# Performance work log

Hardware: AMD Instinct MI355X
Metric: run time of the kernel (lower is better)

Reference implementation:

```python
import jax, jax.numpy as jnp
import numpy as np

B, H, W, C = 512, 7, 7, 768


def _conv3(v, k, b):
    # 1-channel conv1d, kernel size 3, padding 1. v: (B, L), k: (3,), b: scalar
    vp = jnp.pad(v, ((0, 0), (1, 1)))
    return k[0] * vp[:, :-2] + k[1] * vp[:, 1:-1] + k[2] * vp[:, 2:] + b


def setup_inputs() -> dict:
    key = jax.random.key(0)
    ks = jax.random.split(key, 32)
    n = lambda i, shape, s=0.02: jax.random.normal(ks[i], shape, dtype=jnp.float32) * s
    inp = {
        "x": jax.random.normal(ks[0], (B, H, W, C), dtype=jnp.float32),
        # 1x1 Conv2d(dim,dim) weights stored as (out,in)
        "Wh": n(1, (C, C)), "bh": n(2, (C,)),
        "Ww": n(3, (C, C)), "bw": n(4, (C,)),
        "Ws": n(5, (C, C)), "bs": n(6, (C,)),
        # Conv1d(1,1,1) -> scalar weight/bias
        "convH_w": n(7, ()), "convH_b": n(8, ()),
        "convH2_k": n(9, (3,)), "convH2_b": n(10, ()),
        # Conv1d(2,1,1)
        "mixhw_k": n(11, (2,)), "mixhw_b": n(12, ()),
        "mixhw2_k": n(13, (3,)), "mixhw2_b": n(14, ()),
        # Conv1d(3,1,1)
        "mixhws_k": n(15, (3,)), "mixhws_b": n(16, ()),
        "mixhws2_k": n(17, (3,)), "mixhws2_b": n(18, ()),
        # Linear(7, dim)
        "linH_W": n(19, (C, 7), 0.1), "linH_b": n(20, (C,)),
        "linW_W": n(21, (C, 7), 0.1), "linW_b": n(22, (C,)),
        # mix_all: Conv2d(3*dim, dim, 1)
        "mixall_W": n(23, (C, 3 * C)), "mixall_b": n(24, (C,)),
        # proj: Linear(dim, dim)
        "proj_W": n(25, (C, C)), "proj_b": n(26, (C,)),
        "gate_weights": jnp.ones((2,), dtype=jnp.float32),
    }
    return inp


def reference(x, Wh, bh, Ww, bw, Ws, bs, convH_w, convH_b, convH2_k, convH2_b,
              mixhw_k, mixhw_b, mixhw2_k, mixhw2_b, mixhws_k, mixhws_b,
              mixhws2_k, mixhws2_b, linH_W, linH_b, linW_W, linW_b,
              mixall_W, mixall_b, proj_W, proj_b, gate_weights):
    gelu = lambda v: jax.nn.gelu(v, approximate=False)
    sig = jax.nn.sigmoid
    add = x

    # H branch: mlp_h (1x1 conv over channels), pool over (W, C) per H index
    h = gelu(jnp.einsum('bhwc,dc->bhwd', x, Wh) + bh)          # (B,H,W,C)
    h2v = h.mean(axis=(2, 3))                                   # (B,H)
    g_h = sig(_conv3(sig(h2v * convH_w + convH_b), convH2_k, convH2_b))  # (B,H)
    h3 = h * g_h[:, :, None, None]                              # gate per H index

    # W branch: pool over (H, C) per W index, gate mixed with H stats
    w = gelu(jnp.einsum('bhwc,dc->bhwd', x, Ww) + bw)           # (B,H,W,C)
    w2v = w.mean(axis=(1, 3))                                   # (B,W)
    g_hw = sig(_conv3(sig(mixhw_k[0] * h2v + mixhw_k[1] * w2v + mixhw_b),
                      mixhw2_k, mixhw2_b))                      # (B,W)
    w3 = w * g_hw[:, None, :, None]                             # gate per W index

    # C branch: pool over (H, W) per channel, gate mixed with lifted H/W stats
    s = gelu(jnp.einsum('bhwc,dc->bhwd', x, Ws) + bs)           # (B,H,W,C)
    s1v = s.mean(axis=(1, 2))                                   # (B,C)
    h2l = h2v @ linH_W.T + linH_b                               # (B,C)
    w2l = w2v @ linW_W.T + linW_b                               # (B,C)
    g_c = sig(_conv3(sig(mixhws_k[0] * h2l + mixhws_k[1] * w2l
                         + mixhws_k[2] * s1v + mixhws_b),
                     mixhws2_k, mixhws2_b))                     # (B,C)
    s2 = s * g_c[:, None, None, :]                              # gate per channel

    # concat along channel dim + 1x1 mixing conv + proj
    cat = jnp.concatenate([h3, w3, s2], axis=-1)                # (B,H,W,3C)
    mixed = jnp.einsum('bhwk,dk->bhwd', cat, mixall_W) + mixall_b
    out = mixed @ proj_W.T + proj_b
    out = out * gate_weights[0] + add * gate_weights[1]
    return out
```

## Files before the change

### kernel.cpp

```cpp
#include <hip/hip_runtime.h>
#include <cstdint>
#include <cstddef>

typedef __attribute__((ext_vector_type(8))) __bf16 bf16x8;
typedef __attribute__((ext_vector_type(4))) float f32x4;

__device__ __forceinline__ float sigm(float v) { return 1.0f / (1.0f + expf(-v)); }

__device__ __forceinline__ float gelu_fast(float v) {
  float u = v * (1.0f + 0.044715f * v * v);
  float z = 1.5957691216057308f * u;
  return v / (1.0f + __expf(-z));
}

__device__ __forceinline__ void async16(__bf16* lds, const __bf16* g) {
  __builtin_amdgcn_global_load_lds(
      (const __attribute__((address_space(1))) void*)g,
      (__attribute__((address_space(3))) void*)lds, 16, 0, 0);
}

__global__ __launch_bounds__(256) void k_convert(const float* __restrict__ src,
                                                 __bf16* __restrict__ dst, int n8) {
  int i = blockIdx.x * 256 + threadIdx.x;
  if (i >= n8) return;
  const f32x4* s4 = (const f32x4*)src;
  f32x4 a = s4[2 * i], b = s4[2 * i + 1];
  bf16x8 o;
#pragma unroll
  for (int e = 0; e < 4; ++e) { o[e] = (__bf16)a[e]; o[4 + e] = (__bf16)b[e]; }
  ((bf16x8*)dst)[i] = o;
}

__global__ __launch_bounds__(256) void k_bcat(const float* __restrict__ bh,
                                              const float* __restrict__ bw,
                                              const float* __restrict__ bs,
                                              float* __restrict__ bcat) {
  int i = blockIdx.x * 256 + threadIdx.x;
  if (i >= 2304) return;
  bcat[i] = i < 768 ? bh[i] : (i < 1536 ? bw[i - 768] : bs[i - 1536]);
}

__global__ __launch_bounds__(256) void k_transpose_cvt(const float* __restrict__ src,
                                                       __bf16* __restrict__ dst,
                                                       int R, int C) {
  __shared__ float t[32][33];
  const int c0 = blockIdx.x * 32, r0 = blockIdx.y * 32;
  const int tx = threadIdx.x, ty = threadIdx.y;
#pragma unroll
  for (int i = 0; i < 32; i += 8)
    if (r0 + ty + i < R && c0 + tx < C) t[ty + i][tx] = src[(size_t)(r0 + ty + i) * C + c0 + tx];
  __syncthreads();
#pragma unroll
  for (int i = 0; i < 32; i += 8)
    if (c0 + ty + i < C && r0 + tx < R)
      dst[(size_t)(c0 + ty + i) * R + r0 + tx] = (__bf16)t[tx][ty + i];
}

__global__ __launch_bounds__(256) void k_b2(const float* __restrict__ P,
                                            const float* __restrict__ bm,
                                            const float* __restrict__ pb,
                                            float* __restrict__ b2) {
  const int d = blockIdx.x * 256 + threadIdx.x;
  if (d >= 768) return;
  float acc = pb[d];
  const float* row = P + (size_t)d * 768;
#pragma unroll 4
  for (int c = 0; c < 768; c += 4) {
    f32x4 p4 = *(const f32x4*)(row + c);
    f32x4 b4 = *(const f32x4*)(bm + c);
    acc += p4[0] * b4[0] + p4[1] * b4[1] + p4[2] * b4[2] + p4[3] * b4[3];
  }
  b2[d] = acc;
}

template <int EPI>
__global__ __launch_bounds__(256) void k_gemm(
    const __bf16* __restrict__ A, const __bf16* __restrict__ B,
    const float* __restrict__ bias, __bf16* __restrict__ outB,
    float* __restrict__ outF, const float* __restrict__ xres,
    const float* __restrict__ gatew, int N, int K) {
  __shared__ __bf16 lds[16384];
  const int tid = threadIdx.x;
  const int wave = tid >> 6, lane = tid & 63;
  const int nTn = N >> 7;
  const int tm = blockIdx.x / nTn, tn = blockIdx.x % nTn;
  const __bf16* Ag = A + (size_t)tm * 128 * K;
  const __bf16* Bg = B + (size_t)tn * 128 * K;
  const size_t sOff = (size_t)(tid >> 2) * K + ((tid & 3) << 3);

  auto stage = [&](int buf, int t) {
    const int k0 = t << 5;
    __bf16* la = lds + buf * 4096;
    __bf16* lb = lds + 8192 + buf * 4096;
    async16(la + wave * 512,        Ag + sOff + k0);
    async16(la + 2048 + wave * 512, Ag + sOff + (size_t)64 * K + k0);
    async16(lb + wave * 512,        Bg + sOff + k0);
    async16(lb + 2048 + wave * 512, Bg + sOff + (size_t)64 * K + k0);
  };

  f32x4 acc[4][4];
#pragma unroll
  for (int m = 0; m < 4; ++m)
#pragma unroll
    for (int n = 0; n < 4; ++n) acc[m][n] = f32x4{0.f, 0.f, 0.f, 0.f};

  const int wr = wave >> 1, wc = wave & 1;
  const int rb = wr * 64 + (lane & 15);
  const int cb = wc * 64 + (lane & 15);
  const int kf = (lane >> 4) << 3;
  const int nt = K >> 5;

  stage(0, 0);
  __syncthreads();
  int cur = 0;
  for (int t = 0; t < nt; ++t) {
    if (t + 1 < nt) stage(cur ^ 1, t + 1);
    const __bf16* la = lds + cur * 4096;
    const __bf16* lb = lds + 8192 + cur * 4096;
    bf16x8 af[4], bfv[4];
#pragma unroll
    for (int m = 0; m < 4; ++m) af[m] = *(const bf16x8*)&la[(rb + m * 16) * 32 + kf];
#pragma unroll
    for (int n = 0; n < 4; ++n) bfv[n] = *(const bf16x8*)&lb[(cb + n * 16) * 32 + kf];
#pragma unroll
    for (int m = 0; m < 4; ++m)
#pragma unroll
      for (int n = 0; n < 4; ++n)
        acc[m][n] = __builtin_amdgcn_mfma_f32_16x16x32_bf16(af[m], bfv[n], acc[m][n], 0, 0, 0);
    if (t + 1 < nt) __syncthreads();
    cur ^= 1;
  }

  const int orow = (lane >> 4) * 4;
  const int ocol = lane & 15;
  float g0 = 0.f, g1 = 0.f;
  if constexpr (EPI == 2) { g0 = gatew[0]; g1 = gatew[1]; }
#pragma unroll
  for (int m = 0; m < 4; ++m) {
#pragma unroll
    for (int n = 0; n < 4; ++n) {
#pragma unroll
      for (int r = 0; r < 4; ++r) {
        const int rg = tm * 128 + wr * 64 + m * 16 + orow + r;
        const int cg = tn * 128 + wc * 64 + n * 16 + ocol;
        if constexpr (EPI == 0) {
          float v = acc[m][n][r] + bias[cg];
          outB[(size_t)rg * N + cg] = (__bf16)gelu_fast(v);
        } else if constexpr (EPI == 2) {
          float v = acc[m][n][r] + bias[cg];
          outF[(size_t)rg * N + cg] = g0 * v + g1 * xres[(size_t)rg * N + cg];
        } else {
          outB[(size_t)rg * N + cg] = (__bf16)acc[m][n][r];
        }
      }
    }
  }
}

__global__ __launch_bounds__(256) void k_pool(const __bf16* __restrict__ hws,
                                              float* __restrict__ h2v,
                                              float* __restrict__ w2v,
                                              float* __restrict__ s1v) {
  const int b = blockIdx.x, t = threadIdx.x;
  const int lane = t & 63, wave = t >> 6;
  const size_t base = (size_t)b * 49 * 2304;
  float hloc[7], wloc[7];
#pragma unroll
  for (int i = 0; i < 7; ++i) { hloc[i] = 0.f; wloc[i] = 0.f; }
  float sacc[8], sacc2[8];
#pragma unroll
  for (int e = 0; e < 8; ++e) { sacc[e] = 0.f; sacc2[e] = 0.f; }

  const bool isH = t < 96, isW = (t >= 96 && t < 192);
  const int off1 = isH ? t * 8 : (isW ? 768 + (t - 96) * 8 : 1536 + (t - 192) * 8);
  const int off2 = 1536 + (64 + t) * 8;

#pragma unroll
  for (int p = 0; p < 49; ++p) {
    const int hi = p / 7, wi = p % 7;
    const __bf16* row = hws + base + (size_t)p * 2304;
    bf16x8 v = *(const bf16x8*)(row + off1);
    float s8 = 0.f;
#pragma unroll
    for (int e = 0; e < 8; ++e) s8 += (float)v[e];
    if (isH) hloc[hi] += s8;
    else if (isW) wloc[wi] += s8;
    else {
#pragma unroll
      for (int e = 0; e < 8; ++e) sacc[e] += (float)v[e];
    }
    if (t < 32) {
      bf16x8 v2 = *(const bf16x8*)(row + off2);
#pragma unroll
      for (int e = 0; e < 8; ++e) sacc2[e] += (float)v2[e];
    }
  }

  if (t >= 192) {
#pragma unroll
    for (int e = 0; e < 8; ++e)
      s1v[b * 768 + (t - 192) * 8 + e] = sacc[e] * (1.f / 49.f);
  }
  if (t < 32) {
#pragma unroll
    for (int e = 0; e < 8; ++e)
      s1v[b * 768 + 512 + t * 8 + e] = sacc2[e] * (1.f / 49.f);
  }

  __shared__ float red[4][14];
#pragma unroll
  for (int i = 0; i < 7; ++i) {
    float hv = hloc[i], wv = wloc[i];
#pragma unroll
    for (int s = 32; s; s >>= 1) { hv += __shfl_xor(hv, s); wv += __shfl_xor(wv, s); }
    if (lane == 0) { red[wave][i] = hv; red[wave][7 + i] = wv; }
  }
  __syncthreads();
  if (t < 7) {
    h2v[b * 7 + t] = (red[0][t] + red[1][t] + red[2][t] + red[3][t]) * (1.f / 5376.f);
  } else if (t >= 16 && t < 23) {
    const int i = t - 16;
    w2v[b * 7 + i] =
        (red[0][7 + i] + red[1][7 + i] + red[2][7 + i] + red[3][7 + i]) * (1.f / 5376.f);
  }
}

__global__ __launch_bounds__(256) void k_gates(
    const float* __restrict__ h2v, const float* __restrict__ w2v,
    const float* __restrict__ s1v, const float* __restrict__ convH_w,
    const float* __restrict__ convH_b, const float* __restrict__ convH2_k,
    const float* __restrict__ convH2_b, const float* __restrict__ mixhw_k,
    const float* __restrict__ mixhw_b, const float* __restrict__ mixhw2_k,
    const float* __restrict__ mixhw2_b, const float* __restrict__ mixhws_k,
    const float* __restrict__ mixhws_b, const float* __restrict__ mixhws2_k,
    const float* __restrict__ mixhws2_b, const float* __restrict__ linHW,
    const float* __restrict__ linHb, const float* __restrict__ linWW,
    const float* __restrict__ linWb, float* __restrict__ g_h,
    float* __restrict__ g_hw, float* __restrict__ g_c) {
  const int b = blockIdx.x, t = threadIdx.x;
  __shared__ float hv[7], wv[7];
  __shared__ float tc[770];
  if (t < 7) { hv[t] = h2v[b * 7 + t]; wv[t] = w2v[b * 7 + t]; }
  if (t == 7) { tc[0] = 0.f; tc[769] = 0.f; }
  __syncthreads();

  if (t < 7) {
    const float cw = convH_w[0], cbv = convH_b[0];
    const float k0 = convH2_k[0], k1 = convH2_k[1], k2 = convH2_k[2], b2 = convH2_b[0];
    const float um = t > 0 ? sigm(hv[t - 1] * cw + cbv) : 0.f;
    const float u0 = sigm(hv[t] * cw + cbv);
    const float up = t < 6 ? sigm(hv[t + 1] * cw + cbv) : 0.f;
    g_h[b * 7 + t] = sigm(k0 * um + k1 * u0 + k2 * up + b2);

    const float a0 = mixhw_k[0], a1 = mixhw_k[1], ab = mixhw_b[0];
    const float q0 = mixhw2_k[0], q1 = mixhw2_k[1], q2 = mixhw2_k[2], qb = mixhw2_b[0];
    const float vm = t > 0 ? sigm(a0 * hv[t - 1] + a1 * wv[t - 1] + ab) : 0.f;
    const float v0 = sigm(a0 * hv[t] + a1 * wv[t] + ab);
    const float vp = t < 6 ? sigm(a0 * hv[t + 1] + a1 * wv[t + 1] + ab) : 0.f;
    g_hw[b * 7 + t] = sigm(q0 * vm + q1 * v0 + q2 * vp + qb);
  }

  const float m0 = mixhws_k[0], m1 = mixhws_k[1], m2 = mixhws_k[2], mb = mixhws_b[0];
#pragma unroll
  for (int j = 0; j < 3; ++j) {
    const int c = t + j * 256;
    float h2l = linHb[c], w2l = linWb[c];
#pragma unroll
    for (int i = 0; i < 7; ++i) {
      h2l += hv[i] * linHW[c * 7 + i];
      w2l += wv[i] * linWW[c * 7 + i];
    }
    tc[1 + c] = sigm(m0 * h2l + m1 * w2l + m2 * s1v[b * 768 + c] + mb);
  }
  __syncthreads();
  const float r0 = mixhws2_k[0], r1 = mixhws2_k[1], r2 = mixhws2_k[2], rb2 = mixhws2_b[0];
#pragma unroll
  for (int j = 0; j < 3; ++j) {
    const int c = t + j * 256;
    g_c[b * 768 + c] = sigm(r0 * tc[c] + r1 * tc[c + 1] + r2 * tc[c + 2] + rb2);
  }
}

__global__ __launch_bounds__(256) void k_gapply(__bf16* __restrict__ hws,
                                                const float* __restrict__ g_h,
                                                const float* __restrict__ g_hw,
                                                const float* __restrict__ g_c) {
  const int idx = blockIdx.x * 256 + threadIdx.x;
  const int k8 = idx % 288;
  const int p = idx / 288;
  const int b = p / 49, pp = p % 49;
  bf16x8* ptr = (bf16x8*)hws + idx;
  bf16x8 v = *ptr;
  if (k8 < 96) {
    const float g = g_h[b * 7 + pp / 7];
#pragma unroll
    for (int e = 0; e < 8; ++e) v[e] = (__bf16)((float)v[e] * g);
  } else if (k8 < 192) {
    const float g = g_hw[b * 7 + pp % 7];
#pragma unroll
    for (int e = 0; e < 8; ++e) v[e] = (__bf16)((float)v[e] * g);
  } else {
    const float* gcp = g_c + b * 768 + (k8 - 192) * 8;
#pragma unroll
    for (int e = 0; e < 8; ++e) v[e] = (__bf16)((float)v[e] * gcp[e]);
  }
  *ptr = v;
}

extern "C" void kernel_launch(void* const* d_in, const int* in_sizes, int n_in,
                              void* d_out, int out_size, void* d_ws, size_t ws_size,
                              hipStream_t stream) {
  const float* x        = (const float*)d_in[0];
  const float* Wh       = (const float*)d_in[1];
  const float* bh       = (const float*)d_in[2];
  const float* Ww       = (const float*)d_in[3];
  const float* bw       = (const float*)d_in[4];
  const float* Ws       = (const float*)d_in[5];
  const float* bs       = (const float*)d_in[6];
  const float* convH_w  = (const float*)d_in[7];
  const float* convH_b  = (const float*)d_in[8];
  const float* convH2_k = (const float*)d_in[9];
  const float* convH2_b = (const float*)d_in[10];
  const float* mixhw_k  = (const float*)d_in[11];
  const float* mixhw_b  = (const float*)d_in[12];
  const float* mixhw2_k = (const float*)d_in[13];
  const float* mixhw2_b = (const float*)d_in[14];
  const float* mixhws_k = (const float*)d_in[15];
  const float* mixhws_b = (const float*)d_in[16];
  const float* mixhws2_k= (const float*)d_in[17];
  const float* mixhws2_b= (const float*)d_in[18];
  const float* linHW    = (const float*)d_in[19];
  const float* linHb    = (const float*)d_in[20];
  const float* linWW    = (const float*)d_in[21];
  const float* linWb    = (const float*)d_in[22];
  const float* mixallW  = (const float*)d_in[23];
  const float* mixallb  = (const float*)d_in[24];
  const float* projW    = (const float*)d_in[25];
  const float* projb    = (const float*)d_in[26];
  const float* gatew    = (const float*)d_in[27];
  float* out = (float*)d_out;
  (void)in_sizes; (void)n_in; (void)out_size; (void)ws_size;

  const int M = 25088;
  char* ws = (char*)d_ws;
  size_t off = 0;
  auto carve = [&](size_t bytes) -> void* {
    void* p = ws + off;
    off += (bytes + 255) & ~(size_t)255;
    return p;
  };
  __bf16* xb     = (__bf16*)carve((size_t)M * 768 * 2);
  __bf16* Wcat   = (__bf16*)carve((size_t)2304 * 768 * 2);
  __bf16* Pb     = (__bf16*)carve((size_t)768 * 768 * 2);
  __bf16* Dt     = (__bf16*)carve((size_t)2304 * 768 * 2);
  __bf16* W2     = (__bf16*)carve((size_t)768 * 2304 * 2);
  float*  bcat   = (float*)carve(2304 * 4);
  float*  b2     = (float*)carve(768 * 4);
  __bf16* hws    = (__bf16*)carve((size_t)M * 2304 * 2);
  float*  h2v    = (float*)carve(512 * 7 * 4);
  float*  w2v    = (float*)carve(512 * 7 * 4);
  float*  s1v    = (float*)carve(512 * 768 * 4);
  float*  gh     = (float*)carve(512 * 7 * 4);
  float*  ghw    = (float*)carve(512 * 7 * 4);
  float*  gc     = (float*)carve(512 * 768 * 4);

  k_convert<<<9408, 256, 0, stream>>>(x, xb, (M * 768) / 8);
  k_convert<<<288, 256, 0, stream>>>(Wh, Wcat, 73728);
  k_convert<<<288, 256, 0, stream>>>(Ww, Wcat + 589824, 73728);
  k_convert<<<288, 256, 0, stream>>>(Ws, Wcat + 1179648, 73728);
  k_convert<<<288, 256, 0, stream>>>(projW, Pb, 73728);
  k_transpose_cvt<<<dim3(72, 24), dim3(32, 8), 0, stream>>>(mixallW, Dt, 768, 2304);
  k_bcat<<<9, 256, 0, stream>>>(bh, bw, bs, bcat);
  k_b2<<<3, 256, 0, stream>>>(projW, mixallb, projb, b2);

  k_gemm<3><<<6 * 18, 256, 0, stream>>>(Pb, Dt, nullptr, W2, nullptr, nullptr,
                                        nullptr, 2304, 768);
  k_gemm<0><<<196 * 18, 256, 0, stream>>>(xb, Wcat, bcat, hws, nullptr, nullptr,
                                          nullptr, 2304, 768);
  k_pool<<<512, 256, 0, stream>>>(hws, h2v, w2v, s1v);
  k_gates<<<512, 256, 0, stream>>>(h2v, w2v, s1v, convH_w, convH_b, convH2_k,
                                   convH2_b, mixhw_k, mixhw_b, mixhw2_k, mixhw2_b,
                                   mixhws_k, mixhws_b, mixhws2_k, mixhws2_b,
                                   linHW, linHb, linWW, linWb, gh, ghw, gc);
  k_gapply<<<28224, 256, 0, stream>>>(hws, gh, ghw, gc);
  k_gemm<2><<<196 * 6, 256, 0, stream>>>(hws, W2, b2, nullptr, out, x,
                                         gatew, 768, 2304);
}
```

Baseline: 447.6 us.

## Replace 128x128 GEMM with 256x256 tile, 8-wave, swizzled LDS pipelined kernel

Replaces the 128x128 double-buffered GEMM with a 256x256 tile kernel using 512 threads, a K-step of 64, XOR-swizzled LDS layout, and fine-grained interleaving of async global-to-LDS loads with MFMA phases under explicit waitcnt and barriers. It also remaps block IDs so that consecutive tiles land on the same XCD. The aim is higher arithmetic intensity per byte loaded, fewer LDS bank conflicts, and better L2 locality. The cost is much lower grid counts (27, 882 and 294 blocks) with one block per CU, which may underfill the GPU for the small GEMMs, plus fragile hand-written synchronisation.

```diff
diff --git a/kernel.cpp b/kernel.cpp
--- a/kernel.cpp
+++ b/kernel.cpp
@@ -74,61 +74,140 @@
 }
 
 template <int EPI>
-__global__ __launch_bounds__(256) void k_gemm(
+__global__ __launch_bounds__(512, 1) void k_gemm256(
     const __bf16* __restrict__ A, const __bf16* __restrict__ B,
     const float* __restrict__ bias, __bf16* __restrict__ outB,
     float* __restrict__ outF, const float* __restrict__ xres,
     const float* __restrict__ gatew, int N, int K) {
-  __shared__ __bf16 lds[16384];
+  __shared__ __bf16 lds[65536];
   const int tid = threadIdx.x;
-  const int wave = tid >> 6, lane = tid & 63;
-  const int nTn = N >> 7;
-  const int tm = blockIdx.x / nTn, tn = blockIdx.x % nTn;
-  const __bf16* Ag = A + (size_t)tm * 128 * K;
-  const __bf16* Bg = B + (size_t)tn * 128 * K;
-  const size_t sOff = (size_t)(tid >> 2) * K + ((tid & 3) << 3);
-
-  auto stage = [&](int buf, int t) {
-    const int k0 = t << 5;
-    __bf16* la = lds + buf * 4096;
-    __bf16* lb = lds + 8192 + buf * 4096;
-    async16(la + wave * 512,        Ag + sOff + k0);
-    async16(la + 2048 + wave * 512, Ag + sOff + (size_t)64 * K + k0);
-    async16(lb + wave * 512,        Bg + sOff + k0);
-    async16(lb + 2048 + wave * 512, Bg + sOff + (size_t)64 * K + k0);
+  const int lane = tid & 63, wid = tid >> 6;
+  const int wr = wid >> 2, wc = wid & 3;
+
+  const int nwg = gridDim.x;
+  const int q = nwg >> 3, r = nwg & 7;
+  const int xcd = blockIdx.x & 7, idx = blockIdx.x >> 3;
+  const int wgid = (xcd < r ? xcd * (q + 1) : r * (q + 1) + (xcd - r) * q) + idx;
+  const int nTn = N >> 8;
+  const int tm = wgid / nTn, tn = wgid % nTn;
+
+  const __bf16* Ag = A + (size_t)tm * 256 * K;
+  const __bf16* Bg = B + (size_t)tn * 256 * K;
+
+  auto stageH = [&](const __bf16* Og, int base, int kt, int h) {
+#pragma unroll
+    for (int j = 0; j < 2; ++j) {
+      const int lin = j * 512 + tid;
+      const int row = h * 128 + (lin >> 3);
+      const int sc = ((lin & 7) << 3) ^ ((row & 7) << 3);
+      async16(&lds[base + h * 8192 + lin * 8],
+              Og + (size_t)row * K + kt * 64 + sc);
+    }
   };
 
-  f32x4 acc[4][4];
-#pragma unroll
-  for (int m = 0; m < 4; ++m)
+  f32x4 acc[8][4];
+#pragma unroll
+  for (int m = 0; m < 8; ++m)
 #pragma unroll
     for (int n = 0; n < 4; ++n) acc[m][n] = f32x4{0.f, 0.f, 0.f, 0.f};
 
-  const int wr = wave >> 1, wc = wave & 1;
-  const int rb = wr * 64 + (lane & 15);
-  const int cb = wc * 64 + (lane & 15);
-  const int kf = (lane >> 4) << 3;
-  const int nt = K >> 5;
-
-  stage(0, 0);
-  __syncthreads();
-  int cur = 0;
-  for (int t = 0; t < nt; ++t) {
-    if (t + 1 < nt) stage(cur ^ 1, t + 1);
-    const __bf16* la = lds + cur * 4096;
-    const __bf16* lb = lds + 8192 + cur * 4096;
-    bf16x8 af[4], bfv[4];
-#pragma unroll
-    for (int m = 0; m < 4; ++m) af[m] = *(const bf16x8*)&la[(rb + m * 16) * 32 + kf];
-#pragma unroll
-    for (int n = 0; n < 4; ++n) bfv[n] = *(const bf16x8*)&lb[(cb + n * 16) * 32 + kf];
-#pragma unroll
-    for (int m = 0; m < 4; ++m)
-#pragma unroll
-      for (int n = 0; n < 4; ++n)
-        acc[m][n] = __builtin_amdgcn_mfma_f32_16x16x32_bf16(af[m], bfv[n], acc[m][n], 0, 0, 0);
-    if (t + 1 < nt) __syncthreads();
-    cur ^= 1;
+  bf16x8 a[4][2], b[4][2];
+  const int g8 = (lane >> 4) << 3;
+  const int rowA0 = wr * 128 + (lane & 15);
+  const int rowB0 = wc * 64 + (lane & 15);
+
+  auto ldA = [&](int base, int mh) {
+#pragma unroll
+    for (int mm = 0; mm < 4; ++mm) {
+      const int row = rowA0 + (mh * 4 + mm) * 16;
+      const int sw = (row & 7) << 3;
+      const __bf16* p = &lds[base + row * 64];
+      a[mm][0] = *(const bf16x8*)&p[g8 ^ sw];
+      a[mm][1] = *(const bf16x8*)&p[(32 + g8) ^ sw];
+    }
+  };
+  auto ldB2 = [&](int base, int nh) {
+#pragma unroll
+    for (int nn = 0; nn < 2; ++nn) {
+      const int n = nh * 2 + nn;
+      const int row = rowB0 + n * 16;
+      const int sw = (row & 7) << 3;
+      const __bf16* p = &lds[base + row * 64];
+      b[n][0] = *(const bf16x8*)&p[g8 ^ sw];
+      b[n][1] = *(const bf16x8*)&p[(32 + g8) ^ sw];
+    }
+  };
+  auto mma = [&](int mh, int nh) {
+    __builtin_amdgcn_s_setprio(1);
+#pragma unroll
+    for (int mm = 0; mm < 4; ++mm)
+#pragma unroll
+      for (int nn = 0; nn < 2; ++nn) {
+        const int n = nh * 2 + nn, m = mh * 4 + mm;
+        acc[m][n] = __builtin_amdgcn_mfma_f32_16x16x32_bf16(a[mm][0], b[n][0], acc[m][n], 0, 0, 0);
+        acc[m][n] = __builtin_amdgcn_mfma_f32_16x16x32_bf16(a[mm][1], b[n][1], acc[m][n], 0, 0, 0);
+      }
+    __builtin_amdgcn_s_setprio(0);
+  };
+
+  const int NT = K >> 6, NI = NT >> 1;
+
+  stageH(Bg, 32768, 0, 0); stageH(Bg, 32768, 0, 1);
+  stageH(Ag, 0,     0, 0); stageH(Ag, 0,     0, 1);
+  stageH(Bg, 49152, 1, 0); stageH(Bg, 49152, 1, 1);
+  asm volatile("s_waitcnt vmcnt(4)" ::: "memory");
+  __builtin_amdgcn_s_barrier();
+
+  for (int i = 0; i < NI; ++i) {
+    const int T1 = 2 * i + 1;
+    const bool st = (i + 1) < NI;
+    ldA(0, 0); ldB2(32768, 0);
+    stageH(Ag, 16384, T1, 0);
+    __builtin_amdgcn_s_barrier();
+    asm volatile("s_waitcnt lgkmcnt(0)" ::: "memory");
+    mma(0, 0);
+    __builtin_amdgcn_s_barrier();
+    ldB2(32768, 1);
+    stageH(Ag, 16384, T1, 1);
+    __builtin_amdgcn_s_barrier();
+    asm volatile("s_waitcnt lgkmcnt(0)" ::: "memory");
+    mma(0, 1);
+    __builtin_amdgcn_s_barrier();
+    ldA(0, 1);
+    if (st) stageH(Bg, 32768, T1 + 1, 0);
+    __builtin_amdgcn_s_barrier();
+    asm volatile("s_waitcnt lgkmcnt(0)" ::: "memory");
+    mma(1, 0);
+    __builtin_amdgcn_s_barrier();
+    if (st) stageH(Bg, 32768, T1 + 1, 1);
+    __builtin_amdgcn_s_barrier();
+    mma(1, 1);
+    if (st) { asm volatile("s_waitcnt vmcnt(4)" ::: "memory"); }
+    else    { asm volatile("s_waitcnt vmcnt(0)" ::: "memory"); }
+    __builtin_amdgcn_s_barrier();
+    ldA(16384, 0); ldB2(49152, 0);
+    if (st) stageH(Ag, 0, T1 + 1, 0);
+    __builtin_amdgcn_s_barrier();
+    asm volatile("s_waitcnt lgkmcnt(0)" ::: "memory");
+    mma(0, 0);
+    __builtin_amdgcn_s_barrier();
+    ldB2(49152, 1);
+    if (st) stageH(Ag, 0, T1 + 1, 1);
+    __builtin_amdgcn_s_barrier();
+    asm volatile("s_waitcnt lgkmcnt(0)" ::: "memory");
+    mma(0, 1);
+    __builtin_amdgcn_s_barrier();
+    ldA(16384, 1);
+    if (st) stageH(Bg, 49152, T1 + 2, 0);
+    __builtin_amdgcn_s_barrier();
+    asm volatile("s_waitcnt lgkmcnt(0)" ::: "memory");
+    mma(1, 0);
+    __builtin_amdgcn_s_barrier();
+    if (st) stageH(Bg, 49152, T1 + 2, 1);
+    __builtin_amdgcn_s_barrier();
+    mma(1, 1);
+    if (st) { asm volatile("s_waitcnt vmcnt(4)" ::: "memory"); }
+    __builtin_amdgcn_s_barrier();
   }
 
   const int orow = (lane >> 4) * 4;
@@ -136,21 +215,21 @@
   float g0 = 0.f, g1 = 0.f;
   if constexpr (EPI == 2) { g0 = gatew[0]; g1 = gatew[1]; }
 #pragma unroll
-  for (int m = 0; m < 4; ++m) {
+  for (int m = 0; m < 8; ++m) {
 #pragma unroll
     for (int n = 0; n < 4; ++n) {
 #pragma unroll
-      for (int r = 0; r < 4; ++r) {
-        const int rg = tm * 128 + wr * 64 + m * 16 + orow + r;
-        const int cg = tn * 128 + wc * 64 + n * 16 + ocol;
+      for (int rr = 0; rr < 4; ++rr) {
+        const int rg = tm * 256 + wr * 128 + m * 16 + orow + rr;
+        const int cg = tn * 256 + wc * 64 + n * 16 + ocol;
         if constexpr (EPI == 0) {
-          float v = acc[m][n][r] + bias[cg];
+          float v = acc[m][n][rr] + bias[cg];
           outB[(size_t)rg * N + cg] = (__bf16)gelu_fast(v);
         } else if constexpr (EPI == 2) {
-          float v = acc[m][n][r] + bias[cg];
+          float v = acc[m][n][rr] + bias[cg];
           outF[(size_t)rg * N + cg] = g0 * v + g1 * xres[(size_t)rg * N + cg];
         } else {
-          outB[(size_t)rg * N + cg] = (__bf16)acc[m][n][r];
+          outB[(size_t)rg * N + cg] = (__bf16)acc[m][n][rr];
         }
       }
     }
@@ -373,16 +452,16 @@
   k_bcat<<<9, 256, 0, stream>>>(bh, bw, bs, bcat);
   k_b2<<<3, 256, 0, stream>>>(projW, mixallb, projb, b2);
 
-  k_gemm<3><<<6 * 18, 256, 0, stream>>>(Pb, Dt, nullptr, W2, nullptr, nullptr,
-                                        nullptr, 2304, 768);
-  k_gemm<0><<<196 * 18, 256, 0, stream>>>(xb, Wcat, bcat, hws, nullptr, nullptr,
+  k_gemm256<3><<<3 * 9, 512, 0, stream>>>(Pb, Dt, nullptr, W2, nullptr, nullptr,
                                           nullptr, 2304, 768);
+  k_gemm256<0><<<98 * 9, 512, 0, stream>>>(xb, Wcat, bcat, hws, nullptr, nullptr,
+                                           nullptr, 2304, 768);
   k_pool<<<512, 256, 0, stream>>>(hws, h2v, w2v, s1v);
   k_gates<<<512, 256, 0, stream>>>(h2v, w2v, s1v, convH_w, convH_b, convH2_k,
                                    convH2_b, mixhw_k, mixhw_b, mixhw2_k, mixhw2_b,
                                    mixhws_k, mixhws_b, mixhws2_k, mixhws2_b,
                                    linHW, linHb, linWW, linWb, gh, ghw, gc);
   k_gapply<<<28224, 256, 0, stream>>>(hws, gh, ghw, gc);
-  k_gemm<2><<<196 * 6, 256, 0, stream>>>(hws, W2, b2, nullptr, out, x,
-                                         gatew, 768, 2304);
-}
+  k_gemm256<2><<<98 * 3, 512, 0, stream>>>(hws, W2, b2, nullptr, out, x,
+                                           gatew, 768, 2304);
+}
```

Measured after the change: 441.4 us. Within noise of the previous version (-1.4%).

## Restructure GEMM to 256x128 tiles, 3-stage async pipeline, XCD-aware block remap

Applied to the files above, without the earlier changes.

The GEMM kernel moves to 512 threads with 256x128 output tiles and a triple-buffered LDS pipeline. It uses explicit vmcnt waits and raw barriers so two K-slices are in flight at once, and raises MFMA priority with s_setprio. Blocks are also remapped so consecutive tiles land on the same XCD, which aims to improve L2 reuse. The goal is to hide global-load latency and raise MFMA utilisation, at the cost of more LDS per block (72KB) and lower occupancy. The new K-major LDS layout may also bring bank-conflict risk.

```diff
diff --git a/kernel.cpp b/kernel.cpp
--- a/kernel.cpp
+++ b/kernel.cpp
@@ -74,28 +74,36 @@
 }
 
 template <int EPI>
-__global__ __launch_bounds__(256) void k_gemm(
+__global__ __launch_bounds__(512, 4) void k_gemm(
     const __bf16* __restrict__ A, const __bf16* __restrict__ B,
     const float* __restrict__ bias, __bf16* __restrict__ outB,
     float* __restrict__ outF, const float* __restrict__ xres,
     const float* __restrict__ gatew, int N, int K) {
-  __shared__ __bf16 lds[16384];
+  __shared__ __bf16 lds[36864];
   const int tid = threadIdx.x;
-  const int wave = tid >> 6, lane = tid & 63;
+  const int lane = tid & 63, wid = tid >> 6;
+  const int wr = wid >> 1, wc = wid & 1;
+
+  const int nwg = gridDim.x;
+  const int q = nwg >> 3, r = nwg & 7;
+  const int xcd = blockIdx.x & 7, bidx = blockIdx.x >> 3;
+  const int wgid = (xcd < r ? xcd * (q + 1) : r * (q + 1) + (xcd - r) * q) + bidx;
   const int nTn = N >> 7;
-  const int tm = blockIdx.x / nTn, tn = blockIdx.x % nTn;
-  const __bf16* Ag = A + (size_t)tm * 128 * K;
+  const int tm = wgid / nTn, tn = wgid % nTn;
+
+  const __bf16* Ag = A + (size_t)tm * 256 * K;
   const __bf16* Bg = B + (size_t)tn * 128 * K;
-  const size_t sOff = (size_t)(tid >> 2) * K + ((tid & 3) << 3);
-
-  auto stage = [&](int buf, int t) {
-    const int k0 = t << 5;
-    __bf16* la = lds + buf * 4096;
-    __bf16* lb = lds + 8192 + buf * 4096;
-    async16(la + wave * 512,        Ag + sOff + k0);
-    async16(la + 2048 + wave * 512, Ag + sOff + (size_t)64 * K + k0);
-    async16(lb + wave * 512,        Bg + sOff + k0);
-    async16(lb + 2048 + wave * 512, Bg + sOff + (size_t)64 * K + k0);
+
+  auto stage = [&](int buf, int kt) {
+    const int base = buf * 12288;
+#pragma unroll
+    for (int j = 0; j < 2; ++j) {
+      const int lin = j * 512 + tid;
+      async16(&lds[base + lin * 8],
+              Ag + (size_t)(lin & 255) * K + kt * 32 + (lin >> 8) * 8);
+    }
+    async16(&lds[base + 8192 + tid * 8],
+            Bg + (size_t)(tid & 127) * K + kt * 32 + (tid >> 7) * 8);
   };
 
   f32x4 acc[4][4];
@@ -104,31 +112,36 @@
 #pragma unroll
     for (int n = 0; n < 4; ++n) acc[m][n] = f32x4{0.f, 0.f, 0.f, 0.f};
 
-  const int wr = wave >> 1, wc = wave & 1;
-  const int rb = wr * 64 + (lane & 15);
-  const int cb = wc * 64 + (lane & 15);
-  const int kf = (lane >> 4) << 3;
-  const int nt = K >> 5;
+  const int kc = lane >> 4;
+  const int rA = wr * 64 + (lane & 15);
+  const int rB = wc * 64 + (lane & 15);
+  const int NT = K >> 5;
 
   stage(0, 0);
-  __syncthreads();
-  int cur = 0;
-  for (int t = 0; t < nt; ++t) {
-    if (t + 1 < nt) stage(cur ^ 1, t + 1);
-    const __bf16* la = lds + cur * 4096;
-    const __bf16* lb = lds + 8192 + cur * 4096;
+  stage(1, 1);
+  asm volatile("s_waitcnt vmcnt(3)" ::: "memory");
+  __builtin_amdgcn_s_barrier();
+
+  for (int t = 0; t < NT; ++t) {
+    const int cb = (t % 3) * 12288;
+    if (t + 2 < NT) stage((t + 2) % 3, t + 2);
     bf16x8 af[4], bfv[4];
 #pragma unroll
-    for (int m = 0; m < 4; ++m) af[m] = *(const bf16x8*)&la[(rb + m * 16) * 32 + kf];
-#pragma unroll
-    for (int n = 0; n < 4; ++n) bfv[n] = *(const bf16x8*)&lb[(cb + n * 16) * 32 + kf];
+    for (int m = 0; m < 4; ++m)
+      af[m] = *(const bf16x8*)&lds[cb + (kc * 256 + rA + m * 16) * 8];
+#pragma unroll
+    for (int n = 0; n < 4; ++n)
+      bfv[n] = *(const bf16x8*)&lds[cb + 8192 + (kc * 128 + rB + n * 16) * 8];
+    __builtin_amdgcn_s_setprio(1);
 #pragma unroll
     for (int m = 0; m < 4; ++m)
 #pragma unroll
       for (int n = 0; n < 4; ++n)
         acc[m][n] = __builtin_amdgcn_mfma_f32_16x16x32_bf16(af[m], bfv[n], acc[m][n], 0, 0, 0);
-    if (t + 1 < nt) __syncthreads();
-    cur ^= 1;
+    __builtin_amdgcn_s_setprio(0);
+    if (t + 2 < NT) { asm volatile("s_waitcnt vmcnt(3)" ::: "memory"); }
+    else            { asm volatile("s_waitcnt vmcnt(0)" ::: "memory"); }
+    __builtin_amdgcn_s_barrier();
   }
 
   const int orow = (lane >> 4) * 4;
@@ -140,17 +153,17 @@
 #pragma unroll
     for (int n = 0; n < 4; ++n) {
 #pragma unroll
-      for (int r = 0; r < 4; ++r) {
-        const int rg = tm * 128 + wr * 64 + m * 16 + orow + r;
+      for (int rr = 0; rr < 4; ++rr) {
+        const int rg = tm * 256 + wr * 64 + m * 16 + orow + rr;
         const int cg = tn * 128 + wc * 64 + n * 16 + ocol;
         if constexpr (EPI == 0) {
-          float v = acc[m][n][r] + bias[cg];
+          float v = acc[m][n][rr] + bias[cg];
           outB[(size_t)rg * N + cg] = (__bf16)gelu_fast(v);
         } else if constexpr (EPI == 2) {
-          float v = acc[m][n][r] + bias[cg];
+          float v = acc[m][n][rr] + bias[cg];
           outF[(size_t)rg * N + cg] = g0 * v + g1 * xres[(size_t)rg * N + cg];
         } else {
-          outB[(size_t)rg * N + cg] = (__bf16)acc[m][n][r];
+          outB[(size_t)rg * N + cg] = (__bf16)acc[m][n][rr];
         }
       }
     }
@@ -373,16 +386,16 @@
   k_bcat<<<9, 256, 0, stream>>>(bh, bw, bs, bcat);
   k_b2<<<3, 256, 0, stream>>>(projW, mixallb, projb, b2);
 
-  k_gemm<3><<<6 * 18, 256, 0, stream>>>(Pb, Dt, nullptr, W2, nullptr, nullptr,
+  k_gemm<3><<<3 * 18, 512, 0, stream>>>(Pb, Dt, nullptr, W2, nullptr, nullptr,
                                         nullptr, 2304, 768);
-  k_gemm<0><<<196 * 18, 256, 0, stream>>>(xb, Wcat, bcat, hws, nullptr, nullptr,
-                                          nullptr, 2304, 768);
+  k_gemm<0><<<98 * 18, 512, 0, stream>>>(xb, Wcat, bcat, hws, nullptr, nullptr,
+                                         nullptr, 2304, 768);
   k_pool<<<512, 256, 0, stream>>>(hws, h2v, w2v, s1v);
   k_gates<<<512, 256, 0, stream>>>(h2v, w2v, s1v, convH_w, convH_b, convH2_k,
                                    convH2_b, mixhw_k, mixhw_b, mixhw2_k, mixhw2_b,
                                    mixhws_k, mixhws_b, mixhws2_k, mixhws2_b,
                                    linHW, linHb, linWW, linWb, gh, ghw, gc);
   k_gapply<<<28224, 256, 0, stream>>>(hws, gh, ghw, gc);
-  k_gemm<2><<<196 * 6, 256, 0, stream>>>(hws, W2, b2, nullptr, out, x,
-                                         gatew, 768, 2304);
-}
+  k_gemm<2><<<98 * 6, 512, 0, stream>>>(hws, W2, b2, nullptr, out, x,
+                                        gatew, 768, 2304);
+}
```

Result: slower. 631.7 us (+41.1%).
